# Kernel tuning notes

Hardware: AMD Instinct MI355X
Metric: run time of the kernel (lower is better)

The kernel has to match this reference:

```python
import jax, jax.numpy as jnp
import numpy as np

E = 500000       # number of temporal edges
D = 128          # in_feats
DOUT = 128       # out_feats
N_NODES = 50000  # destination node vocabulary


def setup_inputs() -> dict:
    key = jax.random.key(0)
    k = jax.random.split(key, 6)
    src_feat = jax.random.normal(k[0], (E, D), jnp.float32)
    dst_feat = jax.random.normal(k[1], (E, D), jnp.float32)
    # edges sorted by destination node (and implicitly by timestamp within each bucket)
    dst = jnp.sort(jax.random.randint(k[2], (E,), 0, N_NODES))
    W_self = jax.random.normal(k[3], (D, DOUT), jnp.float32) / np.sqrt(D).astype(np.float32)
    b_self = jnp.zeros((DOUT,), jnp.float32)
    W_neigh = jax.random.normal(k[4], (D, DOUT), jnp.float32) / np.sqrt(D).astype(np.float32)
    b_neigh = jnp.zeros((DOUT,), jnp.float32)
    return dict(src_feat=src_feat, dst_feat=dst_feat, dst=dst,
                W_self=W_self, b_self=b_self, W_neigh=W_neigh, b_neigh=b_neigh)


def _segment_cummean(feat, dst):
    """Cumulative mean of `feat` within contiguous buckets of equal `dst`.

    Equivalent to DGL group_apply_edges(group_by='dst') with the 'mean' branch:
    h_feat = cumsum(h_neighs, dim=1) / (deg_index + 1) on the ragged buckets.
    """
    En = feat.shape[0]
    idx = jnp.arange(En)
    is_start = jnp.concatenate([jnp.ones((1,), bool), dst[1:] != dst[:-1]])
    # running max propagates each bucket's start index to all of its edges
    start_idx = jax.lax.associative_scan(jnp.maximum, jnp.where(is_start, idx, 0))
    cs = jnp.cumsum(feat, axis=0)  # [E, D] global prefix sum
    base = jnp.where((start_idx > 0)[:, None],
                     cs[jnp.maximum(start_idx - 1, 0)], jnp.float32(0.0))
    seg_cs = cs - base                       # within-bucket inclusive cumsum
    pos = (idx - start_idx).astype(feat.dtype)
    return seg_cs / (pos + 1.0)[:, None]     # cumulative mean


def reference(src_feat, dst_feat, dst, W_self, b_self, W_neigh, b_neigh):
    h_neigh = _segment_cummean(src_feat, dst)
    # rst = fc_self(h_self) + fc_neigh(mask_feat)
    return (dst_feat @ W_self + b_self) + (h_neigh @ W_neigh + b_neigh)
```

## Files before the change

kernel.cpp:

```cpp
#include <hip/hip_runtime.h>

typedef float f32x4 __attribute__((ext_vector_type(4)));
typedef __bf16 bf16x8 __attribute__((ext_vector_type(8)));

typedef __attribute__((address_space(3))) unsigned char lds_u8;
typedef __attribute__((address_space(1))) const unsigned char g_u8c;

__device__ __forceinline__ unsigned short f2bf(float f) {
  unsigned int u = __float_as_uint(f);
  u += 0x7FFFu + ((u >> 16) & 1u);
  return (unsigned short)(u >> 16);
}
__device__ __forceinline__ bf16x8 cvt8(float4 x, float4 y) {
  bf16x8 r;
  r[0] = (__bf16)x.x; r[1] = (__bf16)x.y; r[2] = (__bf16)x.z; r[3] = (__bf16)x.w;
  r[4] = (__bf16)y.x; r[5] = (__bf16)y.y; r[6] = (__bf16)y.z; r[7] = (__bf16)y.w;
  return r;
}
__device__ __forceinline__ void gload16(const void* g, void* l) {
  __builtin_amdgcn_global_load_lds((g_u8c*)g, (lds_u8*)l, 16, 0, 0);
}

__global__ void k_prep(const float* __restrict__ Ws, const float* __restrict__ Wn,
                       const float* __restrict__ bs, const float* __restrict__ bn,
                       unsigned short* __restrict__ wt, float* __restrict__ bias) {
  int idx = blockIdx.x * 256 + threadIdx.x;
  int n = idx >> 8, k = idx & 255;
  float v = (k < 128) ? Ws[k * 128 + n] : Wn[(k - 128) * 128 + n];
  int ct = n >> 4, l15 = n & 15, kt = k >> 5, lg = (k >> 3) & 3, j = k & 7;
  wt[(((kt << 3) | ct) << 9) + (((lg << 4) | l15) << 3) + j] = f2bf(v);
  if (idx < 128) bias[idx] = bs[idx] + bn[idx];
}

#define SPAN 256

__global__ __launch_bounds__(256) void k_fused(
    const float* __restrict__ src, const float* __restrict__ dstf,
    const int* __restrict__ dst, const unsigned short* __restrict__ wt,
    const float* __restrict__ bias, float* __restrict__ out, int E, int nwg)
{
  __shared__ __align__(16) unsigned char sbuf[2][16384];
  __shared__ __align__(16) unsigned char dbuf[2][16384];
  __shared__ __align__(16) unsigned char ylds[4][2560];
  __shared__ float cbuf[4][128];
  __shared__ unsigned smask[8];
  const int lane = threadIdx.x & 63, wid = threadIdx.x >> 6;
  const int l15 = lane & 15, lg = lane >> 4, l31 = lane & 31;
  const long emax = (long)E - 1;

  const int bid = blockIdx.x;
  const int q = nwg >> 3, r = nwg & 7;
  const int xcd = bid & 7, ix = bid >> 3;
  const int swb = (xcd < r ? xcd * (q + 1) : r * (q + 1) + (xcd - r) * q) + ix;

  const long W0 = (long)swb * SPAN;
  if (W0 >= E) return;
  const long Wend = (W0 + SPAN < (long)E) ? W0 + SPAN : (long)E;
  const int nt = (int)((Wend - W0 + 31) >> 5);

  unsigned char* yw = ylds[wid];
  float* cw = cbuf[wid];
  float bc[2] = { bias[wid * 32 + l15], bias[wid * 32 + 16 + l15] };

  {
    long rc = W0 + threadIdx.x; if (rc > emax) rc = emax;
    long rp = rc - 1; if (rp < 0) rp = 0;
    int dc = dst[rc], dp = dst[rp];
    unsigned long long bal = __ballot((W0 + threadIdx.x > 0) && (dc != dp));
    if (lane == 0) {
      smask[wid * 2]     = (unsigned)(bal & 0xFFFFFFFFull);
      smask[wid * 2 + 1] = (unsigned)(bal >> 32);
    }
  }

  bf16x8 B[8][2];
  #pragma unroll
  for (int kt = 0; kt < 8; ++kt)
    #pragma unroll
    for (int ctt = 0; ctt < 2; ++ctt)
      B[kt][ctt] = *(const bf16x8*)(wt + (((kt << 3) | (wid * 2 + ctt)) << 9) + (lane << 3));

  #pragma unroll
  for (int qd = 0; qd < 4; ++qd) {
    int i = wid * 4 + qd;
    int r2 = i * 2 + (lane >> 5);
    long gr = W0 + r2; if (gr > emax) gr = emax;
    int colb = (l31 << 4) ^ ((r2 & 7) << 4);
    gload16((const char*)src + gr * 512 + colb, sbuf[0] + i * 1024);
    gload16((const char*)dstf + gr * 512 + colb, dbuf[0] + i * 1024);
  }

  int d0 = dst[W0];
  long back = W0 - 1 - lane;
  long backc = back < 0 ? 0 : back;
  int bd = dst[backc];
  unsigned long long mm = __ballot((back >= 0) && (bd == d0));
  unsigned long long nmm = ~mm;
  int L = (nmm == 0ull) ? 64 : __builtin_ctzll(nmm);
  long s = W0 - L;
  while (s > 0 && dst[s - 1] == d0) --s;
  int pos0 = (int)(W0 - s);

  float carry[2] = {0.f, 0.f};
  if (pos0 > 0) {
    float px = 0.f, py = 0.f;
    for (long e = s; e < W0; ) {
      int nb = (int)(W0 - e); if (nb > 8) nb = 8;
      float2 tv[8];
      #pragma unroll
      for (int j = 0; j < 8; ++j)
        if (j < nb) tv[j] = *(const float2*)(src + (e + j) * 128 + lane * 2);
      #pragma unroll
      for (int j = 0; j < 8; ++j)
        if (j < nb) { px += tv[j].x; py += tv[j].y; }
      e += nb;
    }
    cw[lane * 2] = px; cw[lane * 2 + 1] = py;
    asm volatile("s_waitcnt lgkmcnt(0)" ::: "memory");
    #pragma unroll
    for (int ctt = 0; ctt < 2; ++ctt) {
      f32x4 accc = {0.f, 0.f, 0.f, 0.f};
      #pragma unroll
      for (int kt = 0; kt < 4; ++kt) {
        float4 x = {0,0,0,0}, y = {0,0,0,0};
        if (l15 == 0) {
          x = *(const float4*)(cw + kt * 32 + lg * 8);
          y = *(const float4*)(cw + kt * 32 + lg * 8 + 4);
        }
        bf16x8 a = cvt8(x, y);
        accc = __builtin_amdgcn_mfma_f32_16x16x32_bf16(a, B[kt + 4][ctt], accc, 0, 0, 0);
      }
      carry[ctt] = __shfl(accc[0], l15);
    }
  }

  __syncthreads();

  for (int t = 0; t < nt; ++t) {
    const long tb = W0 + (long)t * 32;
    const unsigned char* sb = sbuf[t & 1];
    const unsigned char* db = dbuf[t & 1];
    const unsigned mask = smask[t];

    if (t + 1 < nt) {
      #pragma unroll
      for (int qd = 0; qd < 4; ++qd) {
        int i = wid * 4 + qd;
        int r2 = i * 2 + (lane >> 5);
        long gr = tb + 32 + r2; if (gr > emax) gr = emax;
        int colb = (l31 << 4) ^ ((r2 & 7) << 4);
        gload16((const char*)src + gr * 512 + colb, sbuf[(t + 1) & 1] + i * 1024);
        gload16((const char*)dstf + gr * 512 + colb, dbuf[(t + 1) & 1] + i * 1024);
      }
      asm volatile("" ::: "memory");
    }

    f32x4 accO[2][2] = {{{0,0,0,0},{0,0,0,0}},{{0,0,0,0},{0,0,0,0}}};
    f32x4 accY[2][2] = {{{0,0,0,0},{0,0,0,0}},{{0,0,0,0},{0,0,0,0}}};
    #pragma unroll
    for (int rt = 0; rt < 2; ++rt) {
      int row = rt * 16 + l15;
      const int sw = (row & 7) << 4;
      #pragma unroll
      for (int kt = 0; kt < 4; ++kt) {
        int c0 = kt * 128 + lg * 32;
        float4 sx = *(const float4*)(sb + row * 512 + (c0 ^ sw));
        float4 sy = *(const float4*)(sb + row * 512 + ((c0 + 16) ^ sw));
        float4 dx = *(const float4*)(db + row * 512 + (c0 ^ sw));
        float4 dy = *(const float4*)(db + row * 512 + ((c0 + 16) ^ sw));
        bf16x8 aS = cvt8(sx, sy);
        bf16x8 aD = cvt8(dx, dy);
        #pragma unroll
        for (int ctt = 0; ctt < 2; ++ctt) {
          accO[rt][ctt] = __builtin_amdgcn_mfma_f32_16x16x32_bf16(aD, B[kt][ctt], accO[rt][ctt], 0, 0, 0);
          accY[rt][ctt] = __builtin_amdgcn_mfma_f32_16x16x32_bf16(aS, B[kt + 4][ctt], accY[rt][ctt], 0, 0, 0);
        }
      }
    }

    bf16x8 Mf[2];
    #pragma unroll
    for (int rt = 0; rt < 2; ++rt) {
      int rr = rt * 16 + l15;
      unsigned bits = mask & (0xFFFFFFFFu >> (31 - rr));
      int sr = (bits == 0) ? 0 : (31 - __clz(bits));
      union { unsigned u[4]; bf16x8 v; } mu;
      #pragma unroll
      for (int p = 0; p < 4; ++p) {
        int e0 = lg * 8 + p * 2;
        unsigned lo = (e0 >= sr && e0 <= rr) ? 0x3F80u : 0u;
        unsigned hi = (e0 + 1 >= sr && e0 + 1 <= rr) ? 0x3F80u : 0u;
        mu.u[p] = lo | (hi << 16);
      }
      Mf[rt] = mu.v;
    }

    f32x4 accZ[2][2];
    #pragma unroll
    for (int ctt = 0; ctt < 2; ++ctt) {
      #pragma unroll
      for (int rt = 0; rt < 2; ++rt) {
        unsigned lo = (unsigned)f2bf(accY[rt][ctt][0]) | ((unsigned)f2bf(accY[rt][ctt][1]) << 16);
        unsigned hi = (unsigned)f2bf(accY[rt][ctt][2]) | ((unsigned)f2bf(accY[rt][ctt][3]) << 16);
        *(unsigned long long*)(yw + ctt * 1280 + l15 * 80 + rt * 32 + lg * 8) =
            (unsigned long long)lo | ((unsigned long long)hi << 32);
      }
      asm volatile("s_waitcnt lgkmcnt(0)" ::: "memory");
      bf16x8 yb = *(const bf16x8*)(yw + ctt * 1280 + l15 * 80 + lg * 16);
      #pragma unroll
      for (int rt = 0; rt < 2; ++rt) {
        f32x4 z = {0.f, 0.f, 0.f, 0.f};
        accZ[rt][ctt] = __builtin_amdgcn_mfma_f32_16x16x32_bf16(Mf[rt], yb, z, 0, 0, 0);
      }
    }

    float z31[2];
    #pragma unroll
    for (int ctt = 0; ctt < 2; ++ctt) z31[ctt] = __shfl(accZ[1][ctt][3], 48 + l15);

    #pragma unroll
    for (int rt = 0; rt < 2; ++rt) {
      #pragma unroll
      for (int i = 0; i < 4; ++i) {
        int rr = rt * 16 + lg * 4 + i;
        unsigned bits = mask & (0xFFFFFFFFu >> (31 - rr));
        float cnt, u;
        if (bits == 0) { cnt = (float)(rr + 1 + pos0); u = 1.f; }
        else { cnt = (float)(rr - (31 - __clz(bits)) + 1); u = 0.f; }
        float inv = __builtin_amdgcn_rcpf(cnt);
        long grow = tb + rr;
        if (grow < E) {
          float* op = out + grow * 128 + wid * 32 + l15;
          op[0]  = accO[rt][0][i] + bc[0] + (accZ[rt][0][i] + u * carry[0]) * inv;
          op[16] = accO[rt][1][i] + bc[1] + (accZ[rt][1][i] + u * carry[1]) * inv;
        }
      }
    }

    if (mask == 0) { carry[0] += z31[0]; carry[1] += z31[1]; pos0 += 32; }
    else           { carry[0]  = z31[0]; carry[1]  = z31[1]; pos0 = __clz(mask) + 1; }

    if (t + 1 < nt) {
      asm volatile("s_waitcnt vmcnt(16)" ::: "memory");
      __builtin_amdgcn_s_barrier();
    }
  }
}

extern "C" void kernel_launch(void* const* d_in, const int* in_sizes, int n_in,
                              void* d_out, int out_size, void* d_ws, size_t ws_size,
                              hipStream_t stream) {
  const float* src_feat = (const float*)d_in[0];
  const float* dst_feat = (const float*)d_in[1];
  const int*   dst      = (const int*)d_in[2];
  const float* W_self   = (const float*)d_in[3];
  const float* b_self   = (const float*)d_in[4];
  const float* W_neigh  = (const float*)d_in[5];
  const float* b_neigh  = (const float*)d_in[6];
  float* out = (float*)d_out;
  const int E = in_sizes[2];

  unsigned short* wt   = (unsigned short*)d_ws;
  float*          bias = (float*)((char*)d_ws + 65536);

  k_prep<<<128, 256, 0, stream>>>(W_self, W_neigh, b_self, b_neigh, wt, bias);

  int nwg = (E + SPAN - 1) / SPAN;
  k_fused<<<nwg, 256, 0, stream>>>(src_feat, dst_feat, dst, wt, bias, out, E, nwg);
}
```

Measured before the change: 170.3 us.

## Triple-buffer src tiles, load dst_feat directly to registers, shuffle Y transpose

The dst_feat tile is now read from global memory straight into registers instead of being staged through LDS. The src tile gets a three-stage LDS ring that prefetches two tiles ahead. The bf16 transpose of the Y accumulator used by the masked-prefix MFMA is now done with cross-lane shuffles rather than an LDS round-trip, and the carry scratch reuses a spare sbuf slot. Together these cut LDS use (which may allow higher occupancy) and remove LDS traffic and waits. In exchange, register pressure rises from the 16 float4 dst values held per thread, and the hand-tuned vmcnt counts must match the new load mix.

```diff
diff --git a/kernel.cpp b/kernel.cpp
--- a/kernel.cpp
+++ b/kernel.cpp
@@ -10,6 +10,11 @@
   unsigned int u = __float_as_uint(f);
   u += 0x7FFFu + ((u >> 16) & 1u);
   return (unsigned short)(u >> 16);
+}
+__device__ __forceinline__ unsigned pkbf(float a, float b) {
+  union { __bf16 h[2]; unsigned u; } t;
+  t.h[0] = (__bf16)a; t.h[1] = (__bf16)b;
+  return t.u;
 }
 __device__ __forceinline__ bf16x8 cvt8(float4 x, float4 y) {
   bf16x8 r;
@@ -39,10 +44,7 @@
     const int* __restrict__ dst, const unsigned short* __restrict__ wt,
     const float* __restrict__ bias, float* __restrict__ out, int E, int nwg)
 {
-  __shared__ __align__(16) unsigned char sbuf[2][16384];
-  __shared__ __align__(16) unsigned char dbuf[2][16384];
-  __shared__ __align__(16) unsigned char ylds[4][2560];
-  __shared__ float cbuf[4][128];
+  __shared__ __align__(16) unsigned char sbuf[3][16384];
   __shared__ unsigned smask[8];
   const int lane = threadIdx.x & 63, wid = threadIdx.x >> 6;
   const int l15 = lane & 15, lg = lane >> 4, l31 = lane & 31;
@@ -58,8 +60,6 @@
   const long Wend = (W0 + SPAN < (long)E) ? W0 + SPAN : (long)E;
   const int nt = (int)((Wend - W0 + 31) >> 5);
 
-  unsigned char* yw = ylds[wid];
-  float* cw = cbuf[wid];
   float bc[2] = { bias[wid * 32 + l15], bias[wid * 32 + 16 + l15] };
 
   {
@@ -79,16 +79,6 @@
     #pragma unroll
     for (int ctt = 0; ctt < 2; ++ctt)
       B[kt][ctt] = *(const bf16x8*)(wt + (((kt << 3) | (wid * 2 + ctt)) << 9) + (lane << 3));
-
-  #pragma unroll
-  for (int qd = 0; qd < 4; ++qd) {
-    int i = wid * 4 + qd;
-    int r2 = i * 2 + (lane >> 5);
-    long gr = W0 + r2; if (gr > emax) gr = emax;
-    int colb = (l31 << 4) ^ ((r2 & 7) << 4);
-    gload16((const char*)src + gr * 512 + colb, sbuf[0] + i * 1024);
-    gload16((const char*)dstf + gr * 512 + colb, dbuf[0] + i * 1024);
-  }
 
   int d0 = dst[W0];
   long back = W0 - 1 - lane;
@@ -103,6 +93,7 @@
 
   float carry[2] = {0.f, 0.f};
   if (pos0 > 0) {
+    float* cw = (float*)(sbuf[2] + wid * 512);
     float px = 0.f, py = 0.f;
     for (long e = s; e < W0; ) {
       int nb = (int)(W0 - e); if (nb > 8) nb = 8;
@@ -134,23 +125,56 @@
     }
   }
 
-  __syncthreads();
+  #pragma unroll
+  for (int qd = 0; qd < 4; ++qd) {
+    int i = wid * 4 + qd;
+    int r2 = i * 2 + (lane >> 5);
+    long gr = W0 + r2; if (gr > emax) gr = emax;
+    int colb = (l31 << 4) ^ ((r2 & 7) << 4);
+    gload16((const char*)src + gr * 512 + colb, sbuf[0] + i * 1024);
+  }
+  asm volatile("s_waitcnt lgkmcnt(0)" ::: "memory");
+  if (nt > 1) {
+    #pragma unroll
+    for (int qd = 0; qd < 4; ++qd) {
+      int i = wid * 4 + qd;
+      int r2 = i * 2 + (lane >> 5);
+      long gr = W0 + 32 + r2; if (gr > emax) gr = emax;
+      int colb = (l31 << 4) ^ ((r2 & 7) << 4);
+      gload16((const char*)src + gr * 512 + colb, sbuf[1] + i * 1024);
+    }
+    asm volatile("s_waitcnt vmcnt(4)" ::: "memory");
+  } else {
+    asm volatile("s_waitcnt vmcnt(0)" ::: "memory");
+  }
+  __builtin_amdgcn_s_barrier();
 
   for (int t = 0; t < nt; ++t) {
     const long tb = W0 + (long)t * 32;
-    const unsigned char* sb = sbuf[t & 1];
-    const unsigned char* db = dbuf[t & 1];
+    const unsigned char* sb = sbuf[t % 3];
     const unsigned mask = smask[t];
 
-    if (t + 1 < nt) {
+    float4 df[2][8];
+    #pragma unroll
+    for (int rt = 0; rt < 2; ++rt) {
+      long row = tb + rt * 16 + l15; if (row > emax) row = emax;
+      const float* pd = dstf + row * 128 + lg * 8;
+      #pragma unroll
+      for (int kt = 0; kt < 4; ++kt) {
+        df[rt][kt * 2]     = *(const float4*)(pd + kt * 32);
+        df[rt][kt * 2 + 1] = *(const float4*)(pd + kt * 32 + 4);
+      }
+    }
+    asm volatile("" ::: "memory");
+
+    if (t + 2 < nt) {
       #pragma unroll
       for (int qd = 0; qd < 4; ++qd) {
         int i = wid * 4 + qd;
         int r2 = i * 2 + (lane >> 5);
-        long gr = tb + 32 + r2; if (gr > emax) gr = emax;
+        long gr = tb + 64 + r2; if (gr > emax) gr = emax;
         int colb = (l31 << 4) ^ ((r2 & 7) << 4);
-        gload16((const char*)src + gr * 512 + colb, sbuf[(t + 1) & 1] + i * 1024);
-        gload16((const char*)dstf + gr * 512 + colb, dbuf[(t + 1) & 1] + i * 1024);
+        gload16((const char*)src + gr * 512 + colb, sbuf[(t + 2) % 3] + i * 1024);
       }
       asm volatile("" ::: "memory");
     }
@@ -166,10 +190,8 @@
         int c0 = kt * 128 + lg * 32;
         float4 sx = *(const float4*)(sb + row * 512 + (c0 ^ sw));
         float4 sy = *(const float4*)(sb + row * 512 + ((c0 + 16) ^ sw));
-        float4 dx = *(const float4*)(db + row * 512 + (c0 ^ sw));
-        float4 dy = *(const float4*)(db + row * 512 + ((c0 + 16) ^ sw));
         bf16x8 aS = cvt8(sx, sy);
-        bf16x8 aD = cvt8(dx, dy);
+        bf16x8 aD = cvt8(df[rt][kt * 2], df[rt][kt * 2 + 1]);
         #pragma unroll
         for (int ctt = 0; ctt < 2; ++ctt) {
           accO[rt][ctt] = __builtin_amdgcn_mfma_f32_16x16x32_bf16(aD, B[kt][ctt], accO[rt][ctt], 0, 0, 0);
@@ -198,19 +220,26 @@
     f32x4 accZ[2][2];
     #pragma unroll
     for (int ctt = 0; ctt < 2; ++ctt) {
-      #pragma unroll
-      for (int rt = 0; rt < 2; ++rt) {
-        unsigned lo = (unsigned)f2bf(accY[rt][ctt][0]) | ((unsigned)f2bf(accY[rt][ctt][1]) << 16);
-        unsigned hi = (unsigned)f2bf(accY[rt][ctt][2]) | ((unsigned)f2bf(accY[rt][ctt][3]) << 16);
-        *(unsigned long long*)(yw + ctt * 1280 + l15 * 80 + rt * 32 + lg * 8) =
-            (unsigned long long)lo | ((unsigned long long)hi << 32);
-      }
-      asm volatile("s_waitcnt lgkmcnt(0)" ::: "memory");
-      bf16x8 yb = *(const bf16x8*)(yw + ctt * 1280 + l15 * 80 + lg * 16);
+      unsigned pk00 = pkbf(accY[0][ctt][0], accY[0][ctt][1]);
+      unsigned pk01 = pkbf(accY[0][ctt][2], accY[0][ctt][3]);
+      unsigned pk10 = pkbf(accY[1][ctt][0], accY[1][ctt][1]);
+      unsigned pk11 = pkbf(accY[1][ctt][2], accY[1][ctt][3]);
+      int s0 = l15 + ((lg & 1) ? 32 : 0);
+      int s2 = s0 + 16;
+      unsigned a00 = __shfl(pk00, s0), a01 = __shfl(pk01, s0);
+      unsigned a10 = __shfl(pk10, s0), a11 = __shfl(pk11, s0);
+      unsigned b00 = __shfl(pk00, s2), b01 = __shfl(pk01, s2);
+      unsigned b10 = __shfl(pk10, s2), b11 = __shfl(pk11, s2);
+      bool T = (lg >= 2);
+      union { unsigned u[4]; bf16x8 v; } yu;
+      yu.u[0] = T ? a10 : a00;
+      yu.u[1] = T ? a11 : a01;
+      yu.u[2] = T ? b10 : b00;
+      yu.u[3] = T ? b11 : b01;
       #pragma unroll
       for (int rt = 0; rt < 2; ++rt) {
         f32x4 z = {0.f, 0.f, 0.f, 0.f};
-        accZ[rt][ctt] = __builtin_amdgcn_mfma_f32_16x16x32_bf16(Mf[rt], yb, z, 0, 0, 0);
+        accZ[rt][ctt] = __builtin_amdgcn_mfma_f32_16x16x32_bf16(Mf[rt], yu.v, z, 0, 0, 0);
       }
     }
 
@@ -241,7 +270,8 @@
     else           { carry[0]  = z31[0]; carry[1]  = z31[1]; pos0 = __clz(mask) + 1; }
 
     if (t + 1 < nt) {
-      asm volatile("s_waitcnt vmcnt(16)" ::: "memory");
+      if (t + 2 < nt) asm volatile("s_waitcnt vmcnt(20)" ::: "memory");
+      else            asm volatile("s_waitcnt vmcnt(16)" ::: "memory");
       __builtin_amdgcn_s_barrier();
     }
   }
```

Result: slower. 220.9 us (+29.7%).
